# Kernel optimization log

Hardware: AMD Instinct MI355X
Metric: run time of the kernel (lower is better)

The kernel has to match this reference:

```python
import jax, jax.numpy as jnp
import numpy as np

SIGMA = 1.0  # isotropic Gaussian bandwidth (init kwarg)


def setup_inputs() -> dict:
    key = jax.random.key(0)
    X = jax.random.normal(key, (16384, 64), dtype=jnp.float32)
    return {"X": X}


def reference(X):
    # pairwise squared distances: ||x_i||^2 - 2 x_i.x_j + ||x_j||^2
    sumX2 = jnp.sum(X * X, axis=1, keepdims=True)          # [n, 1]
    D2 = sumX2 - 2.0 * (X @ X.T) + sumX2.T                  # [n, n]
    D2 = jnp.maximum(D2, 0.0)
    K = jnp.exp(-D2 / (2.0 * SIGMA ** 2))
    return K
```

## Files before the change

### kernel.cpp

```cpp
#include <hip/hip_runtime.h>
#include <stdint.h>


typedef __attribute__((ext_vector_type(8))) short s16x8;
typedef __attribute__((ext_vector_type(4))) float f32x4;

#define DDIM 64
#define JT 8
#define LOG2E      1.4426950408889634f
#define HALF_LOG2E 0.7213475204444817f

__device__ inline short cvt1(float x, float& sq) {
  uint32_t u = __builtin_bit_cast(uint32_t, x);
  uint32_t r = (u + 0x7fffu + ((u >> 16) & 1u)) & 0xffff0000u;
  float hf = __builtin_bit_cast(float, r);
  sq += hf * hf;
  return (short)(r >> 16);
}

__device__ inline void issue_row(const float* __restrict__ X, int row, int lq,
                                 f32x4 r[4]) {
  const f32x4* p = reinterpret_cast<const f32x4*>(X + (size_t)row * DDIM + lq * 8);
  const f32x4* q = reinterpret_cast<const f32x4*>(X + (size_t)row * DDIM + 32 + lq * 8);
  r[0] = p[0]; r[1] = p[1]; r[2] = q[0]; r[3] = q[1];
}

__device__ inline void cvt_row(const f32x4 r[4], s16x8 h[2], float& hnorm) {
  float s = 0.f;
#pragma unroll
  for (int ks = 0; ks < 2; ++ks) {
    s16x8 hh;
    hh[0] = cvt1(r[2*ks][0], s);   hh[1] = cvt1(r[2*ks][1], s);
    hh[2] = cvt1(r[2*ks][2], s);   hh[3] = cvt1(r[2*ks][3], s);
    hh[4] = cvt1(r[2*ks+1][0], s); hh[5] = cvt1(r[2*ks+1][1], s);
    hh[6] = cvt1(r[2*ks+1][2], s); hh[7] = cvt1(r[2*ks+1][3], s);
    h[ks] = hh;
  }
  s += __shfl_xor(s, 16);
  s += __shfl_xor(s, 32);
  hnorm = -HALF_LOG2E * s;
}

__global__ __launch_bounds__(256, 2) void gauss_gram_kernel(
    const float* __restrict__ X, float* __restrict__ K, int n) {
  const int lane = threadIdx.x & 63;
  const int wid  = threadIdx.x >> 6;
  const int wr = wid >> 1;
  const int wc = wid & 1;
  const int l15 = lane & 15;
  const int lq  = lane >> 4;

  const int i0     = blockIdx.x * 128 + wr * 64;
  const int jstrip = blockIdx.y * (128 * JT);

  f32x4 araw[4][4];
#pragma unroll
  for (int mi = 0; mi < 4; ++mi)
    issue_row(X, i0 + mi * 16 + l15, lq, araw[mi]);

  f32x4 braw[4][4];
#pragma unroll
  for (int ni = 0; ni < 4; ++ni)
    issue_row(X, jstrip + wc * 64 + ni * 16 + l15, lq, braw[ni]);

  s16x8 a[4][2]; float hA[4];
#pragma unroll
  for (int mi = 0; mi < 4; ++mi)
    cvt_row(araw[mi], a[mi], hA[mi]);

#pragma unroll
  for (int jt = 0; jt < JT; ++jt) {
    const int j0 = jstrip + jt * 128 + wc * 64;

    s16x8 b[4][2]; float hcol[4][4];
#pragma unroll
    for (int ni = 0; ni < 4; ++ni) {
      float hB;
      cvt_row(braw[ni], b[ni], hB);
#pragma unroll
      for (int r = 0; r < 4; ++r)
        hcol[ni][r] = __shfl(hB, lq * 4 + r);
    }

    if (jt + 1 < JT) {
#pragma unroll
      for (int ni = 0; ni < 4; ++ni)
        issue_row(X, jstrip + (jt + 1) * 128 + wc * 64 + ni * 16 + l15, lq, braw[ni]);
    }
    __builtin_amdgcn_sched_barrier(0x2 | 0x4 | 0x8 | 0x1);

    f32x4 acc[4][4] = {};
#pragma unroll
    for (int ks = 0; ks < 2; ++ks)
#pragma unroll
      for (int mi = 0; mi < 4; ++mi)
#pragma unroll
        for (int ni = 0; ni < 4; ++ni)
          acc[mi][ni] = __builtin_amdgcn_mfma_f32_16x16x32_bf16(
              b[ni][ks], a[mi][ks], acc[mi][ni], 0, 0, 0);

#pragma unroll
    for (int mi = 0; mi < 4; ++mi) {
      const int rg = i0 + mi * 16 + l15;
      float* rowp = K + (size_t)rg * n;
#pragma unroll
      for (int ni = 0; ni < 4; ++ni) {
        const int c0 = j0 + ni * 16 + lq * 4;
        f32x4 v;
#pragma unroll
        for (int r = 0; r < 4; ++r) {
          float arg = fminf(hA[mi] + hcol[ni][r] + LOG2E * acc[mi][ni][r], 0.0f);
          float e = exp2f(arg);
          v[r] = (rg == c0 + r) ? 1.0f : e;
        }
        *reinterpret_cast<f32x4*>(rowp + c0) = v;
      }
    }
  }
}

extern "C" void kernel_launch(void* const* d_in, const int* in_sizes, int n_in,
                              void* d_out, int out_size, void* d_ws, size_t ws_size,
                              hipStream_t stream) {
  (void)n_in; (void)d_ws; (void)ws_size; (void)out_size;
  const float* X = (const float*)d_in[0];
  float* K = (float*)d_out;
  const int n = in_sizes[0] / DDIM;
  dim3 grid(n / 128, n / (128 * JT));
  gauss_gram_kernel<<<grid, 256, 0, stream>>>(X, K, n);
}
```

Before: 252.7 us.

## Precompute bf16 X and row norms, then triple-buffer B loads in 8-wave blocks

Adds two prepass kernels that convert X to bf16 in workspace and compute per-row scaled squared norms once. This removes the repeated fp32-to-bf16 conversion and norm reduction that every block did for its B tiles. The main kernel now uses 512-thread blocks with each wave covering 32 columns, and keeps a 3-deep register pipeline of B fragments loaded directly as bf16. The old kernel is kept as a fallback when the workspace is too small. The cost is two extra launches and the workspace traffic.

```diff
diff --git a/kernel.cpp b/kernel.cpp
--- a/kernel.cpp
+++ b/kernel.cpp
@@ -2,13 +2,140 @@
 #include <stdint.h>
 
 
-typedef __attribute__((ext_vector_type(8))) short s16x8;
-typedef __attribute__((ext_vector_type(4))) float f32x4;
+typedef __attribute__((ext_vector_type(8))) short  s16x8;
+typedef __attribute__((ext_vector_type(4))) float  f32x4;
+typedef __attribute__((ext_vector_type(4))) unsigned short u16x4;
 
 #define DDIM 64
 #define JT 8
 #define LOG2E      1.4426950408889634f
 #define HALF_LOG2E 0.7213475204444817f
+
+__device__ inline unsigned short bf16_rne(float x) {
+  uint32_t u = __builtin_bit_cast(uint32_t, x);
+  uint32_t r = (u + 0x7fffu + ((u >> 16) & 1u));
+  return (unsigned short)(r >> 16);
+}
+__device__ inline float bf16_to_f32(unsigned short h) {
+  return __builtin_bit_cast(float, (uint32_t)h << 16);
+}
+
+__global__ __launch_bounds__(256) void k_cvt(const float* __restrict__ X,
+                                             unsigned short* __restrict__ Xb) {
+  int g = blockIdx.x * 256 + threadIdx.x;
+  f32x4 v = reinterpret_cast<const f32x4*>(X)[g];
+  u16x4 h;
+  h[0] = bf16_rne(v[0]); h[1] = bf16_rne(v[1]);
+  h[2] = bf16_rne(v[2]); h[3] = bf16_rne(v[3]);
+  reinterpret_cast<u16x4*>(Xb)[g] = h;
+}
+
+__global__ __launch_bounds__(256) void k_norm(const unsigned short* __restrict__ Xb,
+                                              float* __restrict__ nrm) {
+  int row = blockIdx.x * 256 + threadIdx.x;
+  const s16x8* p = reinterpret_cast<const s16x8*>(Xb + (size_t)row * DDIM);
+  float s = 0.f;
+#pragma unroll
+  for (int k = 0; k < 8; ++k) {
+    s16x8 h = p[k];
+#pragma unroll
+    for (int e = 0; e < 8; ++e) {
+      float f = bf16_to_f32((unsigned short)h[e]);
+      s += f * f;
+    }
+  }
+  nrm[row] = -HALF_LOG2E * s;
+}
+
+__global__ __launch_bounds__(512, 3) void gauss_main(
+    const unsigned short* __restrict__ Xb, const float* __restrict__ nrm,
+    float* __restrict__ K, int n) {
+  const int lane = threadIdx.x & 63;
+  const int wid  = threadIdx.x >> 6;
+  const int wr = wid >> 2;
+  const int wc = wid & 3;
+  const int l15 = lane & 15;
+  const int lq  = lane >> 4;
+
+  const int i0    = blockIdx.x * 128 + wr * 64;
+  const int jbase = blockIdx.y * (128 * JT);
+  const int jw    = wc * 32;
+
+  s16x8 a[4][2];
+  float hA[4];
+#pragma unroll
+  for (int mi = 0; mi < 4; ++mi) {
+    const int row = i0 + mi * 16 + l15;
+#pragma unroll
+    for (int ks = 0; ks < 2; ++ks)
+      a[mi][ks] = *reinterpret_cast<const s16x8*>(
+          Xb + (size_t)row * DDIM + ks * 32 + lq * 8);
+    hA[mi] = nrm[row];
+  }
+
+  s16x8 b[3][2][2];
+  float nb[3];
+#define ISSUE_B(slot, jt_)                                                     \
+  do {                                                                         \
+    const int j0_ = jbase + (jt_) * 128 + jw;                                  \
+    _Pragma("unroll") for (int ni = 0; ni < 2; ++ni) {                         \
+      const int row_ = j0_ + ni * 16 + l15;                                    \
+      _Pragma("unroll") for (int ks = 0; ks < 2; ++ks)                         \
+        b[slot][ni][ks] = *reinterpret_cast<const s16x8*>(                     \
+            Xb + (size_t)row_ * DDIM + ks * 32 + lq * 8);                      \
+    }                                                                          \
+    nb[slot] = nrm[j0_ + (lane & 31)];                                         \
+  } while (0)
+
+  ISSUE_B(0, 0);
+  ISSUE_B(1, 1);
+  ISSUE_B(2, 2);
+
+#pragma unroll
+  for (int jt = 0; jt < JT; ++jt) {
+    const int slot = jt % 3;
+    const int j0 = jbase + jt * 128 + jw;
+
+    float hcol[2][4];
+#pragma unroll
+    for (int ni = 0; ni < 2; ++ni)
+#pragma unroll
+      for (int r = 0; r < 4; ++r)
+        hcol[ni][r] = __shfl(nb[slot], ni * 16 + lq * 4 + r);
+
+    f32x4 acc[4][2] = {};
+#pragma unroll
+    for (int ks = 0; ks < 2; ++ks)
+#pragma unroll
+      for (int mi = 0; mi < 4; ++mi)
+#pragma unroll
+        for (int ni = 0; ni < 2; ++ni)
+          acc[mi][ni] = __builtin_amdgcn_mfma_f32_16x16x32_bf16(
+              b[slot][ni][ks], a[mi][ks], acc[mi][ni], 0, 0, 0);
+
+    if (jt + 3 < JT) ISSUE_B(slot, jt + 3);
+    __builtin_amdgcn_sched_barrier(0x1 | 0x2 | 0x4 | 0x8);
+
+#pragma unroll
+    for (int mi = 0; mi < 4; ++mi) {
+      const int rg = i0 + mi * 16 + l15;
+      float* rowp = K + (size_t)rg * n;
+#pragma unroll
+      for (int ni = 0; ni < 2; ++ni) {
+        const int c0 = j0 + ni * 16 + lq * 4;
+        f32x4 v;
+#pragma unroll
+        for (int r = 0; r < 4; ++r) {
+          float arg = fminf(hA[mi] + hcol[ni][r] + LOG2E * acc[mi][ni][r], 0.0f);
+          float e = exp2f(arg);
+          v[r] = (rg == c0 + r) ? 1.0f : e;
+        }
+        *reinterpret_cast<f32x4*>(rowp + c0) = v;
+      }
+    }
+  }
+#undef ISSUE_B
+}
 
 __device__ inline short cvt1(float x, float& sq) {
   uint32_t u = __builtin_bit_cast(uint32_t, x);
@@ -17,14 +144,12 @@
   sq += hf * hf;
   return (short)(r >> 16);
 }
-
 __device__ inline void issue_row(const float* __restrict__ X, int row, int lq,
                                  f32x4 r[4]) {
   const f32x4* p = reinterpret_cast<const f32x4*>(X + (size_t)row * DDIM + lq * 8);
   const f32x4* q = reinterpret_cast<const f32x4*>(X + (size_t)row * DDIM + 32 + lq * 8);
   r[0] = p[0]; r[1] = p[1]; r[2] = q[0]; r[3] = q[1];
 }
-
 __device__ inline void cvt_row(const f32x4 r[4], s16x8 h[2], float& hnorm) {
   float s = 0.f;
 #pragma unroll
@@ -40,55 +165,41 @@
   s += __shfl_xor(s, 32);
   hnorm = -HALF_LOG2E * s;
 }
-
 __global__ __launch_bounds__(256, 2) void gauss_gram_kernel(
     const float* __restrict__ X, float* __restrict__ K, int n) {
   const int lane = threadIdx.x & 63;
   const int wid  = threadIdx.x >> 6;
-  const int wr = wid >> 1;
-  const int wc = wid & 1;
-  const int l15 = lane & 15;
-  const int lq  = lane >> 4;
-
-  const int i0     = blockIdx.x * 128 + wr * 64;
+  const int wr = wid >> 1, wc = wid & 1;
+  const int l15 = lane & 15, lq = lane >> 4;
+  const int i0 = blockIdx.x * 128 + wr * 64;
   const int jstrip = blockIdx.y * (128 * JT);
-
   f32x4 araw[4][4];
 #pragma unroll
-  for (int mi = 0; mi < 4; ++mi)
-    issue_row(X, i0 + mi * 16 + l15, lq, araw[mi]);
-
+  for (int mi = 0; mi < 4; ++mi) issue_row(X, i0 + mi * 16 + l15, lq, araw[mi]);
   f32x4 braw[4][4];
 #pragma unroll
   for (int ni = 0; ni < 4; ++ni)
     issue_row(X, jstrip + wc * 64 + ni * 16 + l15, lq, braw[ni]);
-
   s16x8 a[4][2]; float hA[4];
 #pragma unroll
-  for (int mi = 0; mi < 4; ++mi)
-    cvt_row(araw[mi], a[mi], hA[mi]);
-
+  for (int mi = 0; mi < 4; ++mi) cvt_row(araw[mi], a[mi], hA[mi]);
 #pragma unroll
   for (int jt = 0; jt < JT; ++jt) {
     const int j0 = jstrip + jt * 128 + wc * 64;
-
     s16x8 b[4][2]; float hcol[4][4];
 #pragma unroll
     for (int ni = 0; ni < 4; ++ni) {
       float hB;
       cvt_row(braw[ni], b[ni], hB);
 #pragma unroll
-      for (int r = 0; r < 4; ++r)
-        hcol[ni][r] = __shfl(hB, lq * 4 + r);
-    }
-
+      for (int r = 0; r < 4; ++r) hcol[ni][r] = __shfl(hB, lq * 4 + r);
+    }
     if (jt + 1 < JT) {
 #pragma unroll
       for (int ni = 0; ni < 4; ++ni)
         issue_row(X, jstrip + (jt + 1) * 128 + wc * 64 + ni * 16 + l15, lq, braw[ni]);
     }
-    __builtin_amdgcn_sched_barrier(0x2 | 0x4 | 0x8 | 0x1);
-
+    __builtin_amdgcn_sched_barrier(0x1 | 0x2 | 0x4 | 0x8);
     f32x4 acc[4][4] = {};
 #pragma unroll
     for (int ks = 0; ks < 2; ++ks)
@@ -98,7 +209,6 @@
         for (int ni = 0; ni < 4; ++ni)
           acc[mi][ni] = __builtin_amdgcn_mfma_f32_16x16x32_bf16(
               b[ni][ks], a[mi][ks], acc[mi][ni], 0, 0, 0);
-
 #pragma unroll
     for (int mi = 0; mi < 4; ++mi) {
       const int rg = i0 + mi * 16 + l15;
@@ -122,10 +232,20 @@
 extern "C" void kernel_launch(void* const* d_in, const int* in_sizes, int n_in,
                               void* d_out, int out_size, void* d_ws, size_t ws_size,
                               hipStream_t stream) {
-  (void)n_in; (void)d_ws; (void)ws_size; (void)out_size;
+  (void)n_in; (void)out_size;
   const float* X = (const float*)d_in[0];
   float* K = (float*)d_out;
   const int n = in_sizes[0] / DDIM;
-  dim3 grid(n / 128, n / (128 * JT));
-  gauss_gram_kernel<<<grid, 256, 0, stream>>>(X, K, n);
-}
+  const size_t need = (size_t)n * DDIM * 2 + (size_t)n * 4;
+  if (ws_size >= need) {
+    unsigned short* Xb = (unsigned short*)d_ws;
+    float* nrm = (float*)((char*)d_ws + (size_t)n * DDIM * 2);
+    k_cvt<<<dim3(n * DDIM / 4 / 256), 256, 0, stream>>>(X, Xb);
+    k_norm<<<dim3(n / 256), 256, 0, stream>>>(Xb, nrm);
+    dim3 grid(n / 128, n / (128 * JT));
+    gauss_main<<<grid, 512, 0, stream>>>(Xb, nrm, K, n);
+  } else {
+    dim3 grid(n / 128, n / (128 * JT));
+    gauss_gram_kernel<<<grid, 256, 0, stream>>>(X, K, n);
+  }
+}
```

New measurement: 269.3 us. 6.6% more time.

## Stage output tiles through LDS for full-row coalesced stores

Applied to the files above, without the earlier changes.

Each block now covers 64 rows by 256 columns per step, with each wave owning 64 columns. Results are written into a padded shared-memory buffer, then read back so every wave stores whole 1 KB row segments of K. The goal is to replace the scattered 16-byte-per-lane stores with fully coalesced row writes on this write-bound kernel. It also drops the fminf clamp and applies the diagonal fixup only on tiles that touch the diagonal. The trade-offs are two barriers per step, about 66 KB of LDS that may limit occupancy, and clamping that no longer happens off the diagonal.

```diff
diff --git a/kernel.cpp b/kernel.cpp
--- a/kernel.cpp
+++ b/kernel.cpp
@@ -7,6 +7,7 @@
 
 #define DDIM 64
 #define JT 8
+#define LROW 260
 #define LOG2E      1.4426950408889634f
 #define HALF_LOG2E 0.7213475204444817f
 
@@ -45,13 +46,14 @@
     const float* __restrict__ X, float* __restrict__ K, int n) {
   const int lane = threadIdx.x & 63;
   const int wid  = threadIdx.x >> 6;
-  const int wr = wid >> 1;
-  const int wc = wid & 1;
   const int l15 = lane & 15;
   const int lq  = lane >> 4;
 
-  const int i0     = blockIdx.x * 128 + wr * 64;
-  const int jstrip = blockIdx.y * (128 * JT);
+  __shared__ float sbuf[64 * LROW];
+
+  const int i0     = blockIdx.x * 64;
+  const int jstrip = blockIdx.y * (256 * JT);
+  const int jw     = wid * 64;
 
   f32x4 araw[4][4];
 #pragma unroll
@@ -61,7 +63,7 @@
   f32x4 braw[4][4];
 #pragma unroll
   for (int ni = 0; ni < 4; ++ni)
-    issue_row(X, jstrip + wc * 64 + ni * 16 + l15, lq, braw[ni]);
+    issue_row(X, jstrip + jw + ni * 16 + l15, lq, braw[ni]);
 
   s16x8 a[4][2]; float hA[4];
 #pragma unroll
@@ -70,7 +72,8 @@
 
 #pragma unroll
   for (int jt = 0; jt < JT; ++jt) {
-    const int j0 = jstrip + jt * 128 + wc * 64;
+    const int jtile = jstrip + jt * 256;
+    const int j0    = jtile + jw;
 
     s16x8 b[4][2]; float hcol[4][4];
 #pragma unroll
@@ -85,9 +88,9 @@
     if (jt + 1 < JT) {
 #pragma unroll
       for (int ni = 0; ni < 4; ++ni)
-        issue_row(X, jstrip + (jt + 1) * 128 + wc * 64 + ni * 16 + l15, lq, braw[ni]);
+        issue_row(X, jstrip + (jt + 1) * 256 + jw + ni * 16 + l15, lq, braw[ni]);
     }
-    __builtin_amdgcn_sched_barrier(0x2 | 0x4 | 0x8 | 0x1);
+    __builtin_amdgcn_sched_barrier(0x1 | 0x2 | 0x4 | 0x8);
 
     f32x4 acc[4][4] = {};
 #pragma unroll
@@ -99,23 +102,43 @@
           acc[mi][ni] = __builtin_amdgcn_mfma_f32_16x16x32_bf16(
               b[ni][ks], a[mi][ks], acc[mi][ni], 0, 0, 0);
 
+    const bool diag = (i0 < j0 + 64) && (j0 < i0 + 64);
+
 #pragma unroll
     for (int mi = 0; mi < 4; ++mi) {
       const int rg = i0 + mi * 16 + l15;
-      float* rowp = K + (size_t)rg * n;
 #pragma unroll
       for (int ni = 0; ni < 4; ++ni) {
         const int c0 = j0 + ni * 16 + lq * 4;
         f32x4 v;
+        if (diag) {
 #pragma unroll
-        for (int r = 0; r < 4; ++r) {
-          float arg = fminf(hA[mi] + hcol[ni][r] + LOG2E * acc[mi][ni][r], 0.0f);
-          float e = exp2f(arg);
-          v[r] = (rg == c0 + r) ? 1.0f : e;
+          for (int r = 0; r < 4; ++r) {
+            float e = exp2f(hA[mi] + hcol[ni][r] + LOG2E * acc[mi][ni][r]);
+            v[r] = (rg == c0 + r) ? 1.0f : e;
+          }
+        } else {
+#pragma unroll
+          for (int r = 0; r < 4; ++r)
+            v[r] = exp2f(hA[mi] + hcol[ni][r] + LOG2E * acc[mi][ni][r]);
         }
-        *reinterpret_cast<f32x4*>(rowp + c0) = v;
+        *reinterpret_cast<f32x4*>(
+            sbuf + (mi * 16 + l15) * LROW + jw + ni * 16 + lq * 4) = v;
       }
     }
+
+    asm volatile("s_waitcnt lgkmcnt(0)" ::: "memory");
+    __builtin_amdgcn_s_barrier();
+
+#pragma unroll
+    for (int r = 0; r < 16; ++r) {
+      const int row = wid * 16 + r;
+      f32x4 t = *reinterpret_cast<const f32x4*>(sbuf + row * LROW + lane * 4);
+      *reinterpret_cast<f32x4*>(K + (size_t)(i0 + row) * n + jtile + lane * 4) = t;
+    }
+
+    asm volatile("s_waitcnt lgkmcnt(0)" ::: "memory");
+    __builtin_amdgcn_s_barrier();
   }
 }
 
@@ -126,6 +149,6 @@
   const float* X = (const float*)d_in[0];
   float* K = (float*)d_out;
   const int n = in_sizes[0] / DDIM;
-  dim3 grid(n / 128, n / (128 * JT));
+  dim3 grid(n / 64, n / (256 * JT));
   gauss_gram_kernel<<<grid, 256, 0, stream>>>(X, K, n);
 }
```

Measured after the change: 384.1 us. +52.0%, slower.
